# Kernel tuning notes

Measured on AMD Instinct MI355X. Metric: run time of the kernel, lower is better.

## Reference

```python
import jax, jax.numpy as jnp
import numpy as np

NUM_GRAPHS = 512
EPS_BN = 1e-5


def _bn(x, g, b):
    # BatchNorm1d in training mode: biased batch statistics over node dim
    m = x.mean(0)
    v = x.var(0)
    return g * (x - m) * jax.lax.rsqrt(v + EPS_BN) + b


def _gcn(x, W, b, src, dst):
    # GCNConv with self-loops and symmetric deg^-1/2 normalization
    n = x.shape[0]
    loop = jnp.arange(n, dtype=src.dtype)
    s = jnp.concatenate([src, loop])
    d = jnp.concatenate([dst, loop])
    h = x @ W  # [N, C_out]
    deg = jax.ops.segment_sum(jnp.ones(d.shape[0], dtype=h.dtype), d, num_segments=n)
    dinv = jax.lax.rsqrt(jnp.maximum(deg, 1.0))  # deg >= 1 due to self-loops
    norm = dinv[s] * dinv[d]  # [E+N]
    out = jax.ops.segment_sum(norm[:, None] * h[s], d, num_segments=n)
    return out + b


def setup_inputs() -> dict:
    key = jax.random.key(0)
    ks = jax.random.split(key, 16)
    N, E, F = 100000, 1600000, 6

    def lin(k, fi, fo):
        k1, k2 = jax.random.split(k)
        s = 1.0 / np.sqrt(fi)
        return (jax.random.uniform(k1, (fi, fo), minval=-s, maxval=s),
                jax.random.uniform(k2, (fo,), minval=-s, maxval=s))

    W1, b1 = lin(ks[0], F, 32)
    W2, b2 = lin(ks[1], 32, 64)
    W3, b3 = lin(ks[2], 64, 128)
    Wf1, bf1 = lin(ks[3], 128, 128)
    Wf2, bf2 = lin(ks[4], 128, 64)
    return {
        "x": jax.random.normal(ks[5], (N, F), dtype=jnp.float32),
        "edge_src": jax.random.randint(ks[6], (E,), 0, N, dtype=jnp.int32),
        "edge_dst": jax.random.randint(ks[7], (E,), 0, N, dtype=jnp.int32),
        "batch": jnp.sort(jax.random.randint(ks[8], (N,), 0, NUM_GRAPHS, dtype=jnp.int32)),
        "W1": W1, "b1": b1, "g1": jnp.ones(32), "be1": jnp.zeros(32),
        "W2": W2, "b2": b2, "g2": jnp.ones(64), "be2": jnp.zeros(64),
        "W3": W3, "b3": b3, "g3": jnp.ones(128), "be3": jnp.zeros(128),
        "Wf1": Wf1, "bf1": bf1, "g4": jnp.ones(128), "be4": jnp.zeros(128),
        "Wf2": Wf2, "bf2": bf2,
    }


def reference(x, edge_src, edge_dst, batch,
              W1, b1, g1, be1, W2, b2, g2, be2, W3, b3, g3, be3,
              Wf1, bf1, g4, be4, Wf2, bf2):
    h = jax.nn.relu(_bn(_gcn(x, W1, b1, edge_src, edge_dst), g1, be1))
    h = jax.nn.relu(_bn(_gcn(h, W2, b2, edge_src, edge_dst), g2, be2))
    h = jax.nn.relu(_bn(_gcn(h, W3, b3, edge_src, edge_dst), g3, be3))
    p = jax.ops.segment_max(h, batch, num_segments=NUM_GRAPHS)  # [G, 128]
    p = jax.nn.relu(_bn(p @ Wf1 + bf1, g4, be4))  # dropout = identity (eval)
    p = p @ Wf2 + bf2
    return p / jnp.maximum(jnp.linalg.norm(p, axis=1, keepdims=True), 1e-12)
```

## Files before the change

### kernel.cpp

```cpp
#include <hip/hip_runtime.h>
#include <hip/hip_bf16.h>
#include <hip/hip_fp16.h>

#define NG 512
#define EPS_BN 1e-5f

__device__ __forceinline__ float4 f4add(float4 a, float4 b) {
    a.x += b.x; a.y += b.y; a.z += b.z; a.w += b.w; return a;
}
__device__ __forceinline__ float4 f4fma(float s, float4 b, float4 a) {
    a.x = fmaf(s, b.x, a.x); a.y = fmaf(s, b.y, a.y);
    a.z = fmaf(s, b.z, a.z); a.w = fmaf(s, b.w, a.w); return a;
}
__device__ __forceinline__ float4 f4max(float4 a, float4 b) {
    a.x = fmaxf(a.x, b.x); a.y = fmaxf(a.y, b.y);
    a.z = fmaxf(a.z, b.z); a.w = fmaxf(a.w, b.w); return a;
}
__device__ __forceinline__ void bnparam(float sm, float sq, float ga, float bt,
                                        float invN, float& sc, float& sh) {
    float m = sm * invN;
    float var = fmaf(-m, m, sq * invN);
    sc = ga * rsqrtf(var + EPS_BN);
    sh = fmaf(-m, sc, bt);
}
__device__ __forceinline__ int enckey(float f) {
    int u = __float_as_int(f);
    return u >= 0 ? u : (u ^ 0x7fffffff);
}
__device__ __forceinline__ float deckey(int k) {
    return __int_as_float(k >= 0 ? k : (k ^ 0x7fffffff));
}
__device__ __forceinline__ void fma_h8(float4 raw, float w, const float* sc,
                                       const float* sh, float* acc) {
    const __half2* hp = reinterpret_cast<const __half2*>(&raw);
#pragma unroll
    for (int i = 0; i < 4; ++i) {
        float2 t = __half22float2(hp[i]);
        acc[2 * i]     = fmaf(w, fmaxf(fmaf(sc[2 * i],     t.x, sh[2 * i]),     0.f), acc[2 * i]);
        acc[2 * i + 1] = fmaf(w, fmaxf(fmaf(sc[2 * i + 1], t.y, sh[2 * i + 1]), 0.f), acc[2 * i + 1]);
    }
}


__global__ void k_count(const int* __restrict__ dst, int* __restrict__ cnt, int E) {
    int i = blockIdx.x * blockDim.x + threadIdx.x;
    if (i < E) atomicAdd(&cnt[dst[i]], 1);
}

__global__ void k_dinv(const int* __restrict__ cnt, float* __restrict__ dinv, int N) {
    int i = blockIdx.x * blockDim.x + threadIdx.x;
    if (i < N) dinv[i] = rsqrtf((float)cnt[i] + 1.0f);
}


#define SCAN_T 256
#define SCAN_I 4

__global__ void k_scan1(const int* __restrict__ in, int* __restrict__ out,
                        int* __restrict__ bsum, int N) {
    __shared__ int lds[SCAN_T];
    int t = threadIdx.x;
    int base = blockIdx.x * (SCAN_T * SCAN_I) + t * SCAN_I;
    int v[SCAN_I];
    int sum = 0;
#pragma unroll
    for (int i = 0; i < SCAN_I; ++i) {
        int idx = base + i;
        v[i] = (idx < N) ? in[idx] : 0;
        sum += v[i];
    }
    lds[t] = sum;
    __syncthreads();
    for (int o = 1; o < SCAN_T; o <<= 1) {
        int a = (t >= o) ? lds[t - o] : 0;
        __syncthreads();
        lds[t] += a;
        __syncthreads();
    }
    int run = lds[t] - sum;
#pragma unroll
    for (int i = 0; i < SCAN_I; ++i) {
        int idx = base + i;
        if (idx < N) out[idx] = run;
        run += v[i];
    }
    if (t == SCAN_T - 1) bsum[blockIdx.x] = lds[SCAN_T - 1];
}

__global__ void k_scan2(int* __restrict__ bs, int nb) {
    __shared__ int lds[SCAN_T];
    int t = threadIdx.x;
    int runbase = 0;
    for (int start = 0; start < nb; start += SCAN_T) {
        int idx = start + t;
        int v = (idx < nb) ? bs[idx] : 0;
        lds[t] = v;
        __syncthreads();
        for (int o = 1; o < SCAN_T; o <<= 1) {
            int a = (t >= o) ? lds[t - o] : 0;
            __syncthreads();
            lds[t] += a;
            __syncthreads();
        }
        if (idx < nb) bs[idx] = runbase + lds[t] - v;
        int tot = lds[SCAN_T - 1];
        __syncthreads();
        runbase += tot;
    }
}

__global__ void k_scan3(int* __restrict__ out, const int* __restrict__ bs, int N) {
    int add = bs[blockIdx.x];
    int base = blockIdx.x * (SCAN_T * SCAN_I) + threadIdx.x * SCAN_I;
#pragma unroll
    for (int i = 0; i < SCAN_I; ++i) {
        int idx = base + i;
        if (idx < N) out[idx] += add;
    }
}


__global__ void k_bucket(const int* __restrict__ src, const int* __restrict__ dst,
                         const float* __restrict__ dinv, const int* __restrict__ rowptr,
                         int* __restrict__ fill, int* __restrict__ esrc,
                         float* __restrict__ ewt, int E) {
    int e = blockIdx.x * blockDim.x + threadIdx.x;
    if (e >= E) return;
    int d = dst[e], s = src[e];
    int pos = rowptr[d] + atomicAdd(&fill[d], 1);
    esrc[pos] = s;
    ewt[pos] = dinv[s];
}


template <int COUT>
__global__ __launch_bounds__(256) void k_layer1(
    const int* __restrict__ rowptr, const int* __restrict__ cnt,
    const int* __restrict__ esrc, const float* __restrict__ ewt,
    const float* __restrict__ dinv, const float* __restrict__ x,
    const float* __restrict__ W, __half* __restrict__ hout,
    float* __restrict__ sums, float* __restrict__ sumsq, int N) {
    constexpr int NPB = 256;
    constexpr int CG = COUT / 4;
    constexpr int RPB = 256 / CG;
    __shared__ float4 inT4[NPB * 6 / 4];
    float* inT = (float*)inT4;
    __shared__ float4 wT[6 * CG];
    __shared__ float4 red[256];
    int t = threadIdx.x;
    const float4* W4 = (const float4*)W;
    for (int i = t; i < 6 * CG; i += 256) wT[i] = W4[i];
    int base = blockIdx.x * NPB;
    int n = base + t;
    if (n < N) {
        const float2* x2 = (const float2*)x;
        int beg = rowptr[n], end = beg + cnt[n];
        float di = dinv[n];
        size_t b3 = (size_t)n * 3;
        float2 p0 = x2[b3], p1 = x2[b3 + 1], p2 = x2[b3 + 2];
        float a0 = di * p0.x, a1 = di * p0.y, a2 = di * p1.x;
        float a3 = di * p1.y, a4 = di * p2.x, a5 = di * p2.y;
        for (int e = beg; e < end; ++e) {
            int s = esrc[e];
            float w = ewt[e];
            size_t s3 = (size_t)s * 3;
            float2 q0 = x2[s3], q1 = x2[s3 + 1], q2 = x2[s3 + 2];
            a0 = fmaf(w, q0.x, a0); a1 = fmaf(w, q0.y, a1);
            a2 = fmaf(w, q1.x, a2); a3 = fmaf(w, q1.y, a3);
            a4 = fmaf(w, q2.x, a4); a5 = fmaf(w, q2.y, a5);
        }
        int o = t * 6;
        inT[o + 0] = di * a0; inT[o + 1] = di * a1; inT[o + 2] = di * a2;
        inT[o + 3] = di * a3; inT[o + 4] = di * a4; inT[o + 5] = di * a5;
    }
    __syncthreads();
    int gi = t % CG, r0 = t / CG, c0 = gi * 4;
    int nrows = min(NPB, N - base);
    float4 s = {0, 0, 0, 0}, s2 = {0, 0, 0, 0};
    for (int r = r0; r < nrows; r += RPB) {
        const float* row = inT + r * 6;
        float4 acc = {0, 0, 0, 0};
#pragma unroll
        for (int k = 0; k < 6; ++k) acc = f4fma(row[k], wT[k * CG + gi], acc);
        union { __half2 h2[2]; uint2 u; } cv;
        cv.h2[0] = __float22half2_rn(make_float2(acc.x, acc.y));
        cv.h2[1] = __float22half2_rn(make_float2(acc.z, acc.w));
        reinterpret_cast<uint2*>(hout)[(size_t)(base + r) * CG + gi] = cv.u;
        s = f4add(s, acc);
        s2.x = fmaf(acc.x, acc.x, s2.x);
        s2.y = fmaf(acc.y, acc.y, s2.y);
        s2.z = fmaf(acc.z, acc.z, s2.z);
        s2.w = fmaf(acc.w, acc.w, s2.w);
    }
    red[t] = s;
    for (int hh = RPB / 2; hh > 0; hh >>= 1) {
        __syncthreads();
        if (r0 < hh) red[t] = f4add(red[t], red[t + hh * CG]);
    }
    if (r0 == 0) {
        float4 a = red[t];
        atomicAdd(&sums[c0 + 0], a.x); atomicAdd(&sums[c0 + 1], a.y);
        atomicAdd(&sums[c0 + 2], a.z); atomicAdd(&sums[c0 + 3], a.w);
    }
    __syncthreads();
    red[t] = s2;
    for (int hh = RPB / 2; hh > 0; hh >>= 1) {
        __syncthreads();
        if (r0 < hh) red[t] = f4add(red[t], red[t + hh * CG]);
    }
    if (r0 == 0) {
        float4 b = red[t];
        atomicAdd(&sumsq[c0 + 0], b.x); atomicAdd(&sumsq[c0 + 1], b.y);
        atomicAdd(&sumsq[c0 + 2], b.z); atomicAdd(&sumsq[c0 + 3], b.w);
    }
}


template <int CIN, int COUT, int NPB, bool SEGMAX>
__global__ __launch_bounds__(256, 6) void k_layerF(
    const int* __restrict__ rowptr, const int* __restrict__ cnt,
    const int* __restrict__ esrc, const float* __restrict__ ewt,
    const float* __restrict__ dinv, const __half* __restrict__ hin,
    const float* __restrict__ sums_in, const float* __restrict__ sumsq_in,
    const float* __restrict__ gam, const float* __restrict__ bet,
    const float* __restrict__ W, __half* __restrict__ hout,
    float* __restrict__ sums_out, float* __restrict__ sumsq_out,
    const int* __restrict__ batch, int* __restrict__ pool,
    int N, float invN) {
    constexpr int TPN = CIN / 8;
    constexpr int PAD = CIN / 4 + 1;
    constexpr int ITER1 = NPB * TPN / 256;
    constexpr int NPI = 256 / TPN;
    constexpr int CG = COUT / 4;
    constexpr int RPB = 256 / CG;
    __shared__ float4 inT4[NPB * PAD];
    __shared__ float4 red[256];
    int t = threadIdx.x;
    int base = blockIdx.x * NPB;
    {
        int c8 = t % TPN;
        float sc[8], sh[8];
        {
            const float4* sm4 = (const float4*)sums_in;
            const float4* sq4 = (const float4*)sumsq_in;
            const float4* ga4 = (const float4*)gam;
            const float4* bt4 = (const float4*)bet;
#pragma unroll
            for (int q = 0; q < 2; ++q) {
                float4 sm = sm4[c8 * 2 + q], sq = sq4[c8 * 2 + q];
                float4 ga = ga4[c8 * 2 + q], bt = bt4[c8 * 2 + q];
                bnparam(sm.x, sq.x, ga.x, bt.x, invN, sc[4 * q + 0], sh[4 * q + 0]);
                bnparam(sm.y, sq.y, ga.y, bt.y, invN, sc[4 * q + 1], sh[4 * q + 1]);
                bnparam(sm.z, sq.z, ga.z, bt.z, invN, sc[4 * q + 2], sh[4 * q + 2]);
                bnparam(sm.w, sq.w, ga.w, bt.w, invN, sc[4 * q + 3], sh[4 * q + 3]);
            }
        }
        const float4* h4 = reinterpret_cast<const float4*>(hin);
#pragma unroll
        for (int it = 0; it < ITER1; ++it) {
            int nl = it * NPI + t / TPN;
            int n = base + nl;
            if (n < N) {
                int beg = rowptr[n], end = beg + cnt[n];
                float di = dinv[n];
                float acc[8] = {0, 0, 0, 0, 0, 0, 0, 0};
                fma_h8(h4[(size_t)n * TPN + c8], di, sc, sh, acc);
                int e = beg;
                for (; e + 3 < end; e += 4) {
                    int s0 = esrc[e], s1 = esrc[e + 1], s2_ = esrc[e + 2], s3_ = esrc[e + 3];
                    float w0 = ewt[e], w1 = ewt[e + 1], w2 = ewt[e + 2], w3 = ewt[e + 3];
                    float4 v0 = h4[(size_t)s0 * TPN + c8];
                    float4 v1 = h4[(size_t)s1 * TPN + c8];
                    float4 v2 = h4[(size_t)s2_ * TPN + c8];
                    float4 v3 = h4[(size_t)s3_ * TPN + c8];
                    fma_h8(v0, w0, sc, sh, acc);
                    fma_h8(v1, w1, sc, sh, acc);
                    fma_h8(v2, w2, sc, sh, acc);
                    fma_h8(v3, w3, sc, sh, acc);
                }
                for (; e < end; ++e)
                    fma_h8(h4[(size_t)esrc[e] * TPN + c8], ewt[e], sc, sh, acc);
                inT4[nl * PAD + 2 * c8] =
                    make_float4(di * acc[0], di * acc[1], di * acc[2], di * acc[3]);
                inT4[nl * PAD + 2 * c8 + 1] =
                    make_float4(di * acc[4], di * acc[5], di * acc[6], di * acc[7]);
            }
        }
    }
    __syncthreads();
    const float4* W4 = (const float4*)W;
    int gi = t % CG, r0 = t / CG, c0 = gi * 4;
    int nrows = min(NPB, N - base);
    float4 s = {0, 0, 0, 0}, s2 = {0, 0, 0, 0};
    int curb = -1;
    float4 mx = {0, 0, 0, 0};
    for (int r = r0; r < nrows; r += RPB) {
        const float* row = (const float*)(inT4 + r * PAD);
        float4 acc = {0, 0, 0, 0};
#pragma unroll 8
        for (int k = 0; k < CIN; ++k) acc = f4fma(row[k], W4[k * CG + gi], acc);
        if constexpr (SEGMAX) {
            int b = batch[base + r];
            if (b != curb) {
                if (curb >= 0) {
                    int* p = pool + (curb << 7) + c0;
                    atomicMax(p + 0, enckey(mx.x)); atomicMax(p + 1, enckey(mx.y));
                    atomicMax(p + 2, enckey(mx.z)); atomicMax(p + 3, enckey(mx.w));
                }
                curb = b; mx = acc;
            } else {
                mx = f4max(mx, acc);
            }
        } else {
            union { __half2 h2[2]; uint2 u; } cv;
            cv.h2[0] = __float22half2_rn(make_float2(acc.x, acc.y));
            cv.h2[1] = __float22half2_rn(make_float2(acc.z, acc.w));
            reinterpret_cast<uint2*>(hout)[(size_t)(base + r) * CG + gi] = cv.u;
        }
        s = f4add(s, acc);
        s2.x = fmaf(acc.x, acc.x, s2.x);
        s2.y = fmaf(acc.y, acc.y, s2.y);
        s2.z = fmaf(acc.z, acc.z, s2.z);
        s2.w = fmaf(acc.w, acc.w, s2.w);
    }
    if constexpr (SEGMAX) {
        if (curb >= 0) {
            int* p = pool + (curb << 7) + c0;
            atomicMax(p + 0, enckey(mx.x)); atomicMax(p + 1, enckey(mx.y));
            atomicMax(p + 2, enckey(mx.z)); atomicMax(p + 3, enckey(mx.w));
        }
    }
    red[t] = s;
    for (int hh = RPB / 2; hh > 0; hh >>= 1) {
        __syncthreads();
        if (r0 < hh) red[t] = f4add(red[t], red[t + hh * CG]);
    }
    if (r0 == 0) {
        float4 a = red[t];
        atomicAdd(&sums_out[c0 + 0], a.x); atomicAdd(&sums_out[c0 + 1], a.y);
        atomicAdd(&sums_out[c0 + 2], a.z); atomicAdd(&sums_out[c0 + 3], a.w);
    }
    __syncthreads();
    red[t] = s2;
    for (int hh = RPB / 2; hh > 0; hh >>= 1) {
        __syncthreads();
        if (r0 < hh) red[t] = f4add(red[t], red[t + hh * CG]);
    }
    if (r0 == 0) {
        float4 b = red[t];
        atomicAdd(&sumsq_out[c0 + 0], b.x); atomicAdd(&sumsq_out[c0 + 1], b.y);
        atomicAdd(&sumsq_out[c0 + 2], b.z); atomicAdd(&sumsq_out[c0 + 3], b.w);
    }
}


__global__ __launch_bounds__(256) void k_mm_pool(
    const int* __restrict__ pool, const float* __restrict__ W,
    const float* __restrict__ sums3, const float* __restrict__ sumsq3,
    const float* __restrict__ g3, const float* __restrict__ be3,
    float* __restrict__ out, float* __restrict__ sums4,
    float* __restrict__ sumsq4, float invN) {
    constexpr int CIN = 128, COUT = 128, ROWS = 64;
    constexpr int CG = COUT / 4;
    constexpr int RPB = 256 / CG;
    __shared__ float4 inT4[ROWS * CIN / 4];
    __shared__ float scA[CIN];
    __shared__ float shA[CIN];
    __shared__ float4 red[256];
    int t = threadIdx.x;
    if (t < CIN) bnparam(sums3[t], sumsq3[t], g3[t], be3[t], invN, scA[t], shA[t]);
    __syncthreads();
    int base = blockIdx.x * ROWS;
    {
        const int4* p4 = reinterpret_cast<const int4*>(pool) + (size_t)base * (CIN / 4);
        for (int i = t; i < ROWS * (CIN / 4); i += 256) {
            int4 k = p4[i];
            int c = (i % (CIN / 4)) * 4;
            float4 v;
            v.x = fmaxf(fmaf(scA[c + 0], deckey(k.x), shA[c + 0]), 0.f);
            v.y = fmaxf(fmaf(scA[c + 1], deckey(k.y), shA[c + 1]), 0.f);
            v.z = fmaxf(fmaf(scA[c + 2], deckey(k.z), shA[c + 2]), 0.f);
            v.w = fmaxf(fmaf(scA[c + 3], deckey(k.w), shA[c + 3]), 0.f);
            inT4[i] = v;
        }
    }
    __syncthreads();
    const float4* W4 = reinterpret_cast<const float4*>(W);
    int gi = t % CG, r0 = t / CG, c0 = gi * 4;
    float4 s = {0, 0, 0, 0}, s2 = {0, 0, 0, 0};
    for (int r = r0; r < ROWS; r += RPB) {
        const float* row = (const float*)(inT4 + r * (CIN / 4));
        float4 acc = {0, 0, 0, 0};
#pragma unroll 8
        for (int k = 0; k < CIN; ++k) acc = f4fma(row[k], W4[k * CG + gi], acc);
        reinterpret_cast<float4*>(out + (size_t)(base + r) * COUT)[gi] = acc;
        s = f4add(s, acc);
        s2.x = fmaf(acc.x, acc.x, s2.x);
        s2.y = fmaf(acc.y, acc.y, s2.y);
        s2.z = fmaf(acc.z, acc.z, s2.z);
        s2.w = fmaf(acc.w, acc.w, s2.w);
    }
    red[t] = s;
    for (int hh = RPB / 2; hh > 0; hh >>= 1) {
        __syncthreads();
        if (r0 < hh) red[t] = f4add(red[t], red[t + hh * CG]);
    }
    if (r0 == 0) {
        float4 a = red[t];
        atomicAdd(&sums4[c0 + 0], a.x); atomicAdd(&sums4[c0 + 1], a.y);
        atomicAdd(&sums4[c0 + 2], a.z); atomicAdd(&sums4[c0 + 3], a.w);
    }
    __syncthreads();
    red[t] = s2;
    for (int hh = RPB / 2; hh > 0; hh >>= 1) {
        __syncthreads();
        if (r0 < hh) red[t] = f4add(red[t], red[t + hh * CG]);
    }
    if (r0 == 0) {
        float4 b = red[t];
        atomicAdd(&sumsq4[c0 + 0], b.x); atomicAdd(&sumsq4[c0 + 1], b.y);
        atomicAdd(&sumsq4[c0 + 2], b.z); atomicAdd(&sumsq4[c0 + 3], b.w);
    }
}


__global__ void k_head(const float* __restrict__ Z, const float* __restrict__ sums,
                       const float* __restrict__ sumsq, const float* __restrict__ gam,
                       const float* __restrict__ bet, const float* __restrict__ Wf2,
                       const float* __restrict__ bf2, float* __restrict__ out) {
    int g = blockIdx.x, c = threadIdx.x;
    __shared__ float row[128];
    const float invG = 1.0f / (float)NG;
    for (int j = c; j < 128; j += 64) {
        float sc, sh;
        bnparam(sums[j], sumsq[j], gam[j], bet[j], invG, sc, sh);
        row[j] = fmaxf(fmaf(sc, Z[(g << 7) + j], sh), 0.f);
    }
    __syncthreads();
    float acc = bf2[c];
#pragma unroll
    for (int k = 0; k < 128; ++k) acc = fmaf(row[k], Wf2[k * 64 + c], acc);
    float ss = acc * acc;
#pragma unroll
    for (int off = 32; off; off >>= 1) ss += __shfl_xor(ss, off);
    out[(g << 6) + c] = acc / fmaxf(sqrtf(ss), 1e-12f);
}


extern "C" void kernel_launch(void* const* d_in, const int* in_sizes, int n_in,
                              void* d_out, int out_size, void* d_ws, size_t ws_size,
                              hipStream_t stream) {
    const float* x    = (const float*)d_in[0];
    const int*   src  = (const int*)d_in[1];
    const int*   dst  = (const int*)d_in[2];
    const int*   batch= (const int*)d_in[3];
    const float* W1   = (const float*)d_in[4];
    const float* g1   = (const float*)d_in[6];
    const float* be1  = (const float*)d_in[7];
    const float* W2   = (const float*)d_in[8];
    const float* g2   = (const float*)d_in[10];
    const float* be2  = (const float*)d_in[11];
    const float* W3   = (const float*)d_in[12];
    const float* g3   = (const float*)d_in[14];
    const float* be3  = (const float*)d_in[15];
    const float* Wf1  = (const float*)d_in[16];
    const float* g4   = (const float*)d_in[18];
    const float* be4  = (const float*)d_in[19];
    const float* Wf2  = (const float*)d_in[20];
    const float* bf2  = (const float*)d_in[21];
    float* out = (float*)d_out;

    const int N = in_sizes[0] / 6;
    const int E = in_sizes[1];
    const int nScanBlocks = (N + SCAN_T * SCAN_I - 1) / (SCAN_T * SCAN_I);

    char* ws = (char*)d_ws;
    size_t off = 0;
    auto carve = [&](size_t bytes) {
        void* p = ws + off;
        off += (bytes + 255) & ~(size_t)255;
        return p;
    };
    int*    cnt    = (int*)carve((size_t)N * 4);
    float*  dinv   = (float*)carve((size_t)N * 4);
    int*    rowptr = (int*)carve((size_t)N * 4);
    int*    fill   = (int*)carve((size_t)N * 4);
    int*    bsum   = (int*)carve((size_t)4096 * 4);
    int*    esrc   = (int*)carve((size_t)E * 4);
    float*  ewt    = (float*)carve((size_t)E * 4);
    __half* H1     = (__half*)carve((size_t)N * 32 * 2);
    __half* H2     = (__half*)carve((size_t)N * 64 * 2);
    float*  stats  = (float*)carve(704 * 4);
    int*    pool   = (int*)carve((size_t)NG * 128 * 4);
    float*  Z      = (float*)carve((size_t)NG * 128 * 4);
    float* s1 = stats;
    float* s2 = stats + 64;
    float* s3 = stats + 192;
    float* s4 = stats + 448;

    const float invN = 1.0f / (float)N;

    hipMemsetAsync(cnt, 0, (size_t)N * 4, stream);
    hipMemsetAsync(fill, 0, (size_t)N * 4, stream);
    hipMemsetAsync(stats, 0, 704 * 4, stream);
    hipMemsetAsync(pool, 0x80, (size_t)NG * 128 * 4, stream);
    k_count<<<(E + 255) / 256, 256, 0, stream>>>(dst, cnt, E);
    k_dinv<<<(N + 255) / 256, 256, 0, stream>>>(cnt, dinv, N);
    k_scan1<<<nScanBlocks, SCAN_T, 0, stream>>>(cnt, rowptr, bsum, N);
    k_scan2<<<1, SCAN_T, 0, stream>>>(bsum, nScanBlocks);
    k_scan3<<<nScanBlocks, SCAN_T, 0, stream>>>(rowptr, bsum, N);
    k_bucket<<<(E + 255) / 256, 256, 0, stream>>>(src, dst, dinv, rowptr, fill, esrc, ewt, E);

    k_layer1<32><<<(N + 255) / 256, 256, 0, stream>>>(
        rowptr, cnt, esrc, ewt, dinv, x, W1, H1, s1, s1 + 32, N);

    k_layerF<32, 64, 64, false><<<(N + 63) / 64, 256, 0, stream>>>(
        rowptr, cnt, esrc, ewt, dinv, H1, s1, s1 + 32, g1, be1, W2, H2,
        s2, s2 + 64, nullptr, nullptr, N, invN);

    k_layerF<64, 128, 64, true><<<(N + 63) / 64, 256, 0, stream>>>(
        rowptr, cnt, esrc, ewt, dinv, H2, s2, s2 + 64, g2, be2, W3, nullptr,
        s3, s3 + 128, batch, pool, N, invN);

    k_mm_pool<<<NG / 64, 256, 0, stream>>>(
        pool, Wf1, s3, s3 + 128, g3, be3, Z, s4, s4 + 128, invN);
    k_head<<<NG, 64, 0, stream>>>(Z, s4, s4 + 128, g4, be4, Wf2, bf2, out);
}
```

Baseline: 825.9 us.

## Split edge aggregation across 16 threads per node with shuffle reduction

Measured after the change: 1.145 ms. 1.39x slower.

```diff
diff --git a/kernel.cpp b/kernel.cpp
--- a/kernel.cpp
+++ b/kernel.cpp
@@ -217,7 +217,7 @@
 
 
 template <int CIN, int COUT, int NPB, bool SEGMAX>
-__global__ __launch_bounds__(256, 6) void k_layerF(
+__global__ __launch_bounds__(256, 8) void k_layerF(
     const int* __restrict__ rowptr, const int* __restrict__ cnt,
     const int* __restrict__ esrc, const float* __restrict__ ewt,
     const float* __restrict__ dinv, const __half* __restrict__ hin,
@@ -228,9 +228,11 @@
     const int* __restrict__ batch, int* __restrict__ pool,
     int N, float invN) {
     constexpr int TPN = CIN / 8;
+    constexpr int ESPLIT = 16 / TPN;
+    constexpr int TPG = 16;
+    constexpr int NPI = 256 / TPG;
+    constexpr int ITER1 = NPB / NPI;
     constexpr int PAD = CIN / 4 + 1;
-    constexpr int ITER1 = NPB * TPN / 256;
-    constexpr int NPI = 256 / TPN;
     constexpr int CG = COUT / 4;
     constexpr int RPB = 256 / CG;
     __shared__ float4 inT4[NPB * PAD];
@@ -238,7 +240,9 @@
     int t = threadIdx.x;
     int base = blockIdx.x * NPB;
     {
-        int c8 = t % TPN;
+        int w = t % TPG;
+        int c8 = w % TPN;
+        int split = w / TPN;
         float sc[8], sh[8];
         {
             const float4* sm4 = (const float4*)sums_in;
@@ -258,32 +262,36 @@
         const float4* h4 = reinterpret_cast<const float4*>(hin);
 #pragma unroll
         for (int it = 0; it < ITER1; ++it) {
-            int nl = it * NPI + t / TPN;
+            int nl = it * NPI + t / TPG;
             int n = base + nl;
             if (n < N) {
                 int beg = rowptr[n], end = beg + cnt[n];
                 float di = dinv[n];
                 float acc[8] = {0, 0, 0, 0, 0, 0, 0, 0};
-                fma_h8(h4[(size_t)n * TPN + c8], di, sc, sh, acc);
-                int e = beg;
-                for (; e + 3 < end; e += 4) {
-                    int s0 = esrc[e], s1 = esrc[e + 1], s2_ = esrc[e + 2], s3_ = esrc[e + 3];
-                    float w0 = ewt[e], w1 = ewt[e + 1], w2 = ewt[e + 2], w3 = ewt[e + 3];
+                if (split == 0)
+                    fma_h8(h4[(size_t)n * TPN + c8], di, sc, sh, acc);
+                int e = beg + split;
+                for (; e + ESPLIT < end; e += 2 * ESPLIT) {
+                    int s0 = esrc[e], s1 = esrc[e + ESPLIT];
+                    float w0 = ewt[e], w1 = ewt[e + ESPLIT];
                     float4 v0 = h4[(size_t)s0 * TPN + c8];
                     float4 v1 = h4[(size_t)s1 * TPN + c8];
-                    float4 v2 = h4[(size_t)s2_ * TPN + c8];
-                    float4 v3 = h4[(size_t)s3_ * TPN + c8];
                     fma_h8(v0, w0, sc, sh, acc);
                     fma_h8(v1, w1, sc, sh, acc);
-                    fma_h8(v2, w2, sc, sh, acc);
-                    fma_h8(v3, w3, sc, sh, acc);
                 }
-                for (; e < end; ++e)
+                if (e < end)
                     fma_h8(h4[(size_t)esrc[e] * TPN + c8], ewt[e], sc, sh, acc);
-                inT4[nl * PAD + 2 * c8] =
-                    make_float4(di * acc[0], di * acc[1], di * acc[2], di * acc[3]);
-                inT4[nl * PAD + 2 * c8 + 1] =
-                    make_float4(di * acc[4], di * acc[5], di * acc[6], di * acc[7]);
+#pragma unroll
+                for (int mask = TPN; mask < TPG; mask <<= 1) {
+#pragma unroll
+                    for (int j = 0; j < 8; ++j) acc[j] += __shfl_xor(acc[j], mask);
+                }
+                if (split == 0) {
+                    inT4[nl * PAD + 2 * c8] =
+                        make_float4(di * acc[0], di * acc[1], di * acc[2], di * acc[3]);
+                    inT4[nl * PAD + 2 * c8 + 1] =
+                        make_float4(di * acc[4], di * acc[5], di * acc[6], di * acc[7]);
+                }
             }
         }
     }
@@ -514,11 +522,11 @@
     k_layer1<32><<<(N + 255) / 256, 256, 0, stream>>>(
         rowptr, cnt, esrc, ewt, dinv, x, W1, H1, s1, s1 + 32, N);
 
-    k_layerF<32, 64, 64, false><<<(N + 63) / 64, 256, 0, stream>>>(
+    k_layerF<32, 64, 32, false><<<(N + 31) / 32, 256, 0, stream>>>(
         rowptr, cnt, esrc, ewt, dinv, H1, s1, s1 + 32, g1, be1, W2, H2,
         s2, s2 + 64, nullptr, nullptr, N, invN);
 
-    k_layerF<64, 128, 64, true><<<(N + 63) / 64, 256, 0, stream>>>(
+    k_layerF<64, 128, 32, true><<<(N + 31) / 32, 256, 0, stream>>>(
         rowptr, cnt, esrc, ewt, dinv, H2, s2, s2 + 64, g2, be2, W3, nullptr,
         s3, s3 + 128, batch, pool, N, invN);
 
```
